# Kernel tuning notes

Hardware: AMD Instinct MI355X
Metric: run time of the kernel (lower is better)

The kernel has to match this reference:

```python
import jax, jax.numpy as jnp
import numpy as np

N_INST = 131072      # total patches across all bags
D_EMB = 512          # VGG16 pooling='max' output dim
ATT_UNITS = 128
CLS_UNITS = 512
NUM_BAGS = 256


def setup_inputs() -> dict:
    key = jax.random.key(0)
    ks = jax.random.split(key, 16)
    first_emb = jax.random.normal(ks[0], (N_INST, D_EMB), dtype=jnp.float32)
    first_lab = jnp.sort(jax.random.randint(ks[1], (N_INST,), 0, NUM_BAGS)).astype(jnp.int64)
    s = 0.02
    return {
        "first_emb": first_emb,
        "first_lab": first_lab,
        # first-level attention head: Dense(tanh) -> Dense(1, sigmoid)
        "W_a1": jax.random.normal(ks[2], (D_EMB, ATT_UNITS), dtype=jnp.float32) * s,
        "b_a1": jnp.zeros((ATT_UNITS,), dtype=jnp.float32),
        "w_o1": jax.random.normal(ks[3], (ATT_UNITS, 1), dtype=jnp.float32) * s,
        "b_o1": jnp.zeros((1,), dtype=jnp.float32),
        # second-level attention head
        "W_a2": jax.random.normal(ks[4], (D_EMB, ATT_UNITS), dtype=jnp.float32) * s,
        "b_a2": jnp.zeros((ATT_UNITS,), dtype=jnp.float32),
        "w_o2": jax.random.normal(ks[5], (ATT_UNITS, 1), dtype=jnp.float32) * s,
        "b_o2": jnp.zeros((1,), dtype=jnp.float32),
        # classifier: Dense(CLS_UNITS, linear) -> Dense(1, sigmoid)
        "W_c": jax.random.normal(ks[6], (D_EMB, CLS_UNITS), dtype=jnp.float32) * s,
        "b_c": jnp.zeros((CLS_UNITS,), dtype=jnp.float32),
        "w_out": jax.random.normal(ks[7], (CLS_UNITS, 1), dtype=jnp.float32) * s,
        "b_out": jnp.zeros((1,), dtype=jnp.float32),
    }


def reference(first_emb, first_lab, W_a1, b_a1, w_o1, b_o1,
              W_a2, b_a2, w_o2, b_o2, W_c, b_c, w_out, b_out):
    # --- first-level (instance) attention ---
    a1 = jnp.tanh(first_emb @ W_a1 + b_a1)                 # [N, A]
    att1 = jax.nn.sigmoid(a1 @ w_o1 + b_o1)                # [N, 1]
    # tf: transpose(softmax(transpose(att))) == softmax over the N axis (global)
    fst_att = jax.nn.softmax(att1, axis=0)                 # [N, 1]
    # --- per-bag attention-weighted sum (fused segment reduce) ---
    # replaces the python loop of gather_nd + matmul over contiguous bags
    second_emb = jax.ops.segment_sum(fst_att * first_emb, first_lab,
                                     num_segments=NUM_BAGS)  # [B, D]
    # --- second-level (bag) attention ---
    a2 = jnp.tanh(second_emb @ W_a2 + b_a2)                # [B, A]
    att2 = jax.nn.sigmoid(a2 @ w_o2 + b_o2)                # [B, 1]
    snd_att = jax.nn.softmax(att2.T, axis=-1)              # [1, B]
    outer_bag_emb = snd_att @ second_emb                   # [1, D]
    # --- classifier (dropout is identity at inference) ---
    h = outer_bag_emb @ W_c + b_c                          # [1, CLS]
    pred = jax.nn.sigmoid(h @ w_out + b_out)               # [1, 1]
    return pred
```

## Files before the change

kernel.cpp:

```cpp
#include <hip/hip_runtime.h>
#include <cstdint>
#include <cstddef>

#define N_INST 131072
#define D_EMB  512
#define ATT    128
#define NBAGS  256
#define TILE_I 64
#define LDA    520

typedef __attribute__((ext_vector_type(8))) short  bf16x8;
typedef __attribute__((ext_vector_type(4))) float  f32x4;
typedef __attribute__((ext_vector_type(4))) unsigned short u16x4;


__device__ inline unsigned short f2b(float f) {
    unsigned u = __builtin_bit_cast(unsigned, f);
    u += 0x7FFFu + ((u >> 16) & 1u);
    return (unsigned short)(u >> 16);
}

__global__ __launch_bounds__(256) void k_prep_wt(
    const float* __restrict__ Wa1, unsigned short* __restrict__ Wt)
{
    const int n = blockIdx.x;
    for (int k = threadIdx.x; k < D_EMB; k += 256)
        Wt[(size_t)n * D_EMB + k] = f2b(Wa1[(size_t)k * ATT + n]);
}

__global__ __launch_bounds__(256, 2) void k_att1(
    const float* __restrict__ emb, const int* __restrict__ lab,
    const unsigned short* __restrict__ Wt, const float* __restrict__ ba1,
    const float* __restrict__ wo1, const float* __restrict__ bo1,
    float* __restrict__ raw, float* __restrict__ Z1)
{
    __shared__ unsigned short Ash[TILE_I * LDA];
    __shared__ float att[TILE_I];
    __shared__ float sval[TILE_I];
    __shared__ int   labs[TILE_I];

    const int t  = threadIdx.x;
    const int w  = t >> 6;
    const int l  = t & 63;
    const int l4 = l & 15;
    const int h4 = l >> 4;
    const size_t i0 = (size_t)blockIdx.x * TILE_I;

    if (t < TILE_I) { labs[t] = lab[i0 + t]; att[t] = 0.f; }

    bf16x8 bfrag[2][16];
    #pragma unroll
    for (int nt = 0; nt < 2; ++nt) {
        const int n = 16 * (2 * w + nt) + l4;
        #pragma unroll
        for (int ks = 0; ks < 16; ++ks)
            bfrag[nt][ks] = *reinterpret_cast<const bf16x8*>(
                &Wt[(size_t)n * D_EMB + 32 * ks + 8 * h4]);
    }

    float ba1v[2], wo1v[2];
    #pragma unroll
    for (int nt = 0; nt < 2; ++nt) {
        int c = 16 * (2 * w + nt) + l4;
        ba1v[nt] = ba1[c];
        wo1v[nt] = wo1[c];
    }

    #pragma unroll
    for (int g = 0; g < 4; ++g) {
        float4 v[8];
        #pragma unroll
        for (int j = 0; j < 8; ++j) {
            int idx = (g * 8 + j) * 256 + t;
            int row = idx >> 7;
            int c4  = (idx & 127) * 4;
            v[j] = *reinterpret_cast<const float4*>(&emb[(i0 + row) * D_EMB + c4]);
        }
        #pragma unroll
        for (int j = 0; j < 8; ++j) {
            int idx = (g * 8 + j) * 256 + t;
            int row = idx >> 7;
            int c4  = (idx & 127) * 4;
            u16x4 b = { f2b(v[j].x), f2b(v[j].y), f2b(v[j].z), f2b(v[j].w) };
            *reinterpret_cast<u16x4*>(&Ash[row * LDA + c4]) = b;
        }
    }
    __syncthreads();

    f32x4 acc[4][2];
    #pragma unroll
    for (int rt = 0; rt < 4; ++rt) {
        acc[rt][0] = (f32x4){0.f, 0.f, 0.f, 0.f};
        acc[rt][1] = (f32x4){0.f, 0.f, 0.f, 0.f};
    }
    #pragma unroll
    for (int rt = 0; rt < 4; ++rt) {
        #pragma unroll
        for (int ks = 0; ks < 16; ++ks) {
            bf16x8 af = *reinterpret_cast<const bf16x8*>(
                &Ash[(16 * rt + l4) * LDA + 32 * ks + 8 * h4]);
            acc[rt][0] = __builtin_amdgcn_mfma_f32_16x16x32_bf16(
                af, bfrag[0][ks], acc[rt][0], 0, 0, 0);
            acc[rt][1] = __builtin_amdgcn_mfma_f32_16x16x32_bf16(
                af, bfrag[1][ks], acc[rt][1], 0, 0, 0);
        }
    }

    #pragma unroll
    for (int rt = 0; rt < 4; ++rt) {
        #pragma unroll
        for (int reg = 0; reg < 4; ++reg) {
            float p = tanhf(acc[rt][0][reg] + ba1v[0]) * wo1v[0]
                    + tanhf(acc[rt][1][reg] + ba1v[1]) * wo1v[1];
            p += __shfl_xor(p, 1);
            p += __shfl_xor(p, 2);
            p += __shfl_xor(p, 4);
            p += __shfl_xor(p, 8);
            if (l4 == 0) atomicAdd(&att[16 * rt + 4 * h4 + reg], p);
        }
    }
    __syncthreads();
    if (t < TILE_I) {
        float a  = att[t] + bo1[0];
        float sg = 1.f / (1.f + __expf(-a));
        sval[t]  = __expf(sg);
    }
    __syncthreads();
    if (t < TILE_I) {
        float z = sval[t];
        #pragma unroll
        for (int m = 1; m < 64; m <<= 1) z += __shfl_xor(z, m);
        if (t == 0) atomicAdd(Z1, z);
    }

    int s0 = 0;
    while (s0 < TILE_I) {
        int bag = labs[s0];
        int s1 = s0 + 1;
        while (s1 < TILE_I && labs[s1] == bag) ++s1;
        float a0 = 0.f, a1 = 0.f;
        #pragma unroll 8
        for (int ii = s0; ii < s1; ++ii) {
            unsigned u = *reinterpret_cast<const unsigned*>(
                &Ash[(size_t)ii * LDA + 2 * t]);
            float lo = __builtin_bit_cast(float, u << 16);
            float hi = __builtin_bit_cast(float, u & 0xffff0000u);
            float s  = sval[ii];
            a0 = fmaf(s, lo, a0);
            a1 = fmaf(s, hi, a1);
        }
        atomicAdd(&raw[bag * D_EMB + 2 * t], a0);
        atomicAdd(&raw[bag * D_EMB + 2 * t + 1], a1);
        s0 = s1;
    }
}

__global__ __launch_bounds__(128) void k_att2(
    const float* __restrict__ Wa2, const float* __restrict__ ba2,
    const float* __restrict__ wo2, const float* __restrict__ bo2,
    float* __restrict__ raw, const float* __restrict__ Z1,
    float* __restrict__ e2, float* __restrict__ Z2)
{
    __shared__ float sec[D_EMB];
    __shared__ float hh[2];
    const int b = blockIdx.x;
    const int t = threadIdx.x;
    const float zinv = 1.f / Z1[0];
    for (int d = t; d < D_EMB; d += 128) {
        float v = raw[b * D_EMB + d] * zinv;
        raw[b * D_EMB + d] = v;
        sec[d] = v;
    }
    __syncthreads();
    float dot = 0.f;
    #pragma unroll 8
    for (int d = 0; d < D_EMB; ++d) dot = fmaf(sec[d], Wa2[d * ATT + t], dot);
    float h = tanhf(dot + ba2[t]) * wo2[t];
    #pragma unroll
    for (int m = 1; m < 64; m <<= 1) h += __shfl_xor(h, m);
    if ((t & 63) == 0) hh[t >> 6] = h;
    __syncthreads();
    if (t == 0) {
        float a  = hh[0] + hh[1] + bo2[0];
        float sg = 1.f / (1.f + __expf(-a));
        float e  = __expf(sg);
        e2[b] = e;
        atomicAdd(Z2, e);
    }
}

__global__ __launch_bounds__(256) void k_v(
    const float* __restrict__ Wc, const float* __restrict__ wout,
    float* __restrict__ v)
{
    const int t   = threadIdx.x;
    const int row = blockIdx.x * 8 + (t >> 5);
    const int l   = t & 31;
    float s = 0.f;
    #pragma unroll 4
    for (int c = l; c < 512; c += 32) s = fmaf(Wc[(size_t)row * 512 + c], wout[c], s);
    #pragma unroll
    for (int m = 1; m < 32; m <<= 1) s += __shfl_xor(s, m);
    if (l == 0) v[row] = s;
}

__global__ __launch_bounds__(256) void k_pool(
    const float* __restrict__ raw, const float* __restrict__ e2,
    float* __restrict__ outer)
{
    const int t  = threadIdx.x;
    const int b0 = blockIdx.x * 32;
    float o0 = 0.f, o1 = 0.f;
    for (int b = b0; b < b0 + 32; ++b) {
        float wgt = e2[b];
        float2 r = *reinterpret_cast<const float2*>(&raw[b * D_EMB + 2 * t]);
        o0 = fmaf(wgt, r.x, o0);
        o1 = fmaf(wgt, r.y, o1);
    }
    atomicAdd(&outer[2 * t], o0);
    atomicAdd(&outer[2 * t + 1], o1);
}

__global__ __launch_bounds__(256) void k_cls(
    const float* __restrict__ outer, const float* __restrict__ Z2,
    const float* __restrict__ v, const float* __restrict__ bc,
    const float* __restrict__ wout, const float* __restrict__ bout,
    float* __restrict__ out)
{
    __shared__ float pp[4];
    const int t = threadIdx.x;
    const float z2inv = 1.f / Z2[0];
    float p = (outer[2 * t] * v[2 * t] + outer[2 * t + 1] * v[2 * t + 1]) * z2inv
            + bc[2 * t] * wout[2 * t] + bc[2 * t + 1] * wout[2 * t + 1];
    #pragma unroll
    for (int m = 1; m < 64; m <<= 1) p += __shfl_xor(p, m);
    if ((t & 63) == 0) pp[t >> 6] = p;
    __syncthreads();
    if (t == 0) {
        float s = pp[0] + pp[1] + pp[2] + pp[3] + bout[0];
        out[0] = 1.f / (1.f + __expf(-s));
    }
}

extern "C" void kernel_launch(void* const* d_in, const int* in_sizes, int n_in,
                              void* d_out, int out_size, void* d_ws, size_t ws_size,
                              hipStream_t stream)
{
    const float* emb  = (const float*)d_in[0];
    const int*   lab  = (const int*)d_in[1];
    const float* Wa1  = (const float*)d_in[2];
    const float* ba1  = (const float*)d_in[3];
    const float* wo1  = (const float*)d_in[4];
    const float* bo1  = (const float*)d_in[5];
    const float* Wa2  = (const float*)d_in[6];
    const float* ba2  = (const float*)d_in[7];
    const float* wo2  = (const float*)d_in[8];
    const float* bo2  = (const float*)d_in[9];
    const float* Wc   = (const float*)d_in[10];
    const float* bc   = (const float*)d_in[11];
    const float* wout = (const float*)d_in[12];
    const float* bout = (const float*)d_in[13];

    float* ws    = (float*)d_ws;
    float* Z1    = ws + 0;
    float* Z2    = ws + 1;
    float* v     = ws + 16;
    float* e2    = ws + 1024;
    float* outer = ws + 1536;
    float* raw   = ws + 2048;
    unsigned short* Wt = (unsigned short*)(ws + 133120);

    hipMemsetAsync(d_ws, 0, (size_t)(2048 + NBAGS * D_EMB) * sizeof(float), stream);

    hipLaunchKernelGGL(k_prep_wt, dim3(ATT),             dim3(256), 0, stream, Wa1, Wt);
    hipLaunchKernelGGL(k_v,       dim3(64),              dim3(256), 0, stream, Wc, wout, v);
    hipLaunchKernelGGL(k_att1,    dim3(N_INST / TILE_I), dim3(256), 0, stream,
                       emb, lab, Wt, ba1, wo1, bo1, raw, Z1);
    hipLaunchKernelGGL(k_att2,    dim3(NBAGS),           dim3(128), 0, stream,
                       Wa2, ba2, wo2, bo2, raw, Z1, e2, Z2);
    hipLaunchKernelGGL(k_pool,    dim3(8),               dim3(256), 0, stream,
                       raw, e2, outer);
    hipLaunchKernelGGL(k_cls,     dim3(1),               dim3(256), 0, stream,
                       outer, Z2, v, bc, wout, bout, (float*)d_out);
}
```

Before: 140.3 us.

## Replicate per-bag accumulators to cut atomic contention, use fast tanh

```diff
diff --git a/kernel.cpp b/kernel.cpp
--- a/kernel.cpp
+++ b/kernel.cpp
@@ -20,6 +20,11 @@
     return (unsigned short)(u >> 16);
 }
 
+__device__ inline float fast_tanh(float x) {
+    float e = __expf(2.f * x);
+    return 1.f - 2.f / (e + 1.f);
+}
+
 __global__ __launch_bounds__(256) void k_prep_wt(
     const float* __restrict__ Wa1, unsigned short* __restrict__ Wt)
 {
@@ -32,10 +37,10 @@
     const float* __restrict__ emb, const int* __restrict__ lab,
     const unsigned short* __restrict__ Wt, const float* __restrict__ ba1,
     const float* __restrict__ wo1, const float* __restrict__ bo1,
-    float* __restrict__ raw, float* __restrict__ Z1)
+    float* __restrict__ rawr, int R, float* __restrict__ Z1)
 {
     __shared__ unsigned short Ash[TILE_I * LDA];
-    __shared__ float att[TILE_I];
+    __shared__ float att4[4][TILE_I];
     __shared__ float sval[TILE_I];
     __shared__ int   labs[TILE_I];
 
@@ -45,8 +50,9 @@
     const int l4 = l & 15;
     const int h4 = l >> 4;
     const size_t i0 = (size_t)blockIdx.x * TILE_I;
-
-    if (t < TILE_I) { labs[t] = lab[i0 + t]; att[t] = 0.f; }
+    float* __restrict__ raw = rawr + (size_t)(blockIdx.x % R) * (NBAGS * D_EMB);
+
+    if (t < TILE_I) labs[t] = lab[i0 + t];
 
     bf16x8 bfrag[2][16];
     #pragma unroll
@@ -67,18 +73,18 @@
     }
 
     #pragma unroll
-    for (int g = 0; g < 4; ++g) {
-        float4 v[8];
-        #pragma unroll
-        for (int j = 0; j < 8; ++j) {
-            int idx = (g * 8 + j) * 256 + t;
+    for (int g = 0; g < 2; ++g) {
+        float4 v[16];
+        #pragma unroll
+        for (int j = 0; j < 16; ++j) {
+            int idx = (g * 16 + j) * 256 + t;
             int row = idx >> 7;
             int c4  = (idx & 127) * 4;
             v[j] = *reinterpret_cast<const float4*>(&emb[(i0 + row) * D_EMB + c4]);
         }
         #pragma unroll
-        for (int j = 0; j < 8; ++j) {
-            int idx = (g * 8 + j) * 256 + t;
+        for (int j = 0; j < 16; ++j) {
+            int idx = (g * 16 + j) * 256 + t;
             int row = idx >> 7;
             int c4  = (idx & 127) * 4;
             u16x4 b = { f2b(v[j].x), f2b(v[j].y), f2b(v[j].z), f2b(v[j].w) };
@@ -110,18 +116,18 @@
     for (int rt = 0; rt < 4; ++rt) {
         #pragma unroll
         for (int reg = 0; reg < 4; ++reg) {
-            float p = tanhf(acc[rt][0][reg] + ba1v[0]) * wo1v[0]
-                    + tanhf(acc[rt][1][reg] + ba1v[1]) * wo1v[1];
+            float p = fast_tanh(acc[rt][0][reg] + ba1v[0]) * wo1v[0]
+                    + fast_tanh(acc[rt][1][reg] + ba1v[1]) * wo1v[1];
             p += __shfl_xor(p, 1);
             p += __shfl_xor(p, 2);
             p += __shfl_xor(p, 4);
             p += __shfl_xor(p, 8);
-            if (l4 == 0) atomicAdd(&att[16 * rt + 4 * h4 + reg], p);
+            if (l4 == 0) att4[w][16 * rt + 4 * h4 + reg] = p;
         }
     }
     __syncthreads();
     if (t < TILE_I) {
-        float a  = att[t] + bo1[0];
+        float a  = att4[0][t] + att4[1][t] + att4[2][t] + att4[3][t] + bo1[0];
         float sg = 1.f / (1.f + __expf(-a));
         sval[t]  = __expf(sg);
     }
@@ -158,7 +164,7 @@
 __global__ __launch_bounds__(128) void k_att2(
     const float* __restrict__ Wa2, const float* __restrict__ ba2,
     const float* __restrict__ wo2, const float* __restrict__ bo2,
-    float* __restrict__ raw, const float* __restrict__ Z1,
+    float* __restrict__ rawr, int R, const float* __restrict__ Z1,
     float* __restrict__ e2, float* __restrict__ Z2)
 {
     __shared__ float sec[D_EMB];
@@ -167,15 +173,18 @@
     const int t = threadIdx.x;
     const float zinv = 1.f / Z1[0];
     for (int d = t; d < D_EMB; d += 128) {
-        float v = raw[b * D_EMB + d] * zinv;
-        raw[b * D_EMB + d] = v;
+        float s = 0.f;
+        for (int r = 0; r < R; ++r)
+            s += rawr[(size_t)r * (NBAGS * D_EMB) + b * D_EMB + d];
+        float v = s * zinv;
+        rawr[b * D_EMB + d] = v;
         sec[d] = v;
     }
     __syncthreads();
     float dot = 0.f;
     #pragma unroll 8
     for (int d = 0; d < D_EMB; ++d) dot = fmaf(sec[d], Wa2[d * ATT + t], dot);
-    float h = tanhf(dot + ba2[t]) * wo2[t];
+    float h = fast_tanh(dot + ba2[t]) * wo2[t];
     #pragma unroll
     for (int m = 1; m < 64; m <<= 1) h += __shfl_xor(h, m);
     if ((t & 63) == 0) hh[t >> 6] = h;
@@ -267,19 +276,22 @@
     float* v     = ws + 16;
     float* e2    = ws + 1024;
     float* outer = ws + 1536;
-    float* raw   = ws + 2048;
-    unsigned short* Wt = (unsigned short*)(ws + 133120);
-
-    hipMemsetAsync(d_ws, 0, (size_t)(2048 + NBAGS * D_EMB) * sizeof(float), stream);
+    unsigned short* Wt = (unsigned short*)(ws + 4096);
+    float* rawr  = ws + 36864;
+
+    const size_t need8 = ((size_t)36864 + 8u * NBAGS * D_EMB) * sizeof(float);
+    const int R = (ws_size >= need8) ? 8 : 1;
+
+    hipMemsetAsync(d_ws, 0, ((size_t)36864 + (size_t)R * NBAGS * D_EMB) * sizeof(float), stream);
 
     hipLaunchKernelGGL(k_prep_wt, dim3(ATT),             dim3(256), 0, stream, Wa1, Wt);
     hipLaunchKernelGGL(k_v,       dim3(64),              dim3(256), 0, stream, Wc, wout, v);
     hipLaunchKernelGGL(k_att1,    dim3(N_INST / TILE_I), dim3(256), 0, stream,
-                       emb, lab, Wt, ba1, wo1, bo1, raw, Z1);
+                       emb, lab, Wt, ba1, wo1, bo1, rawr, R, Z1);
     hipLaunchKernelGGL(k_att2,    dim3(NBAGS),           dim3(128), 0, stream,
-                       Wa2, ba2, wo2, bo2, raw, Z1, e2, Z2);
+                       Wa2, ba2, wo2, bo2, rawr, R, Z1, e2, Z2);
     hipLaunchKernelGGL(k_pool,    dim3(8),               dim3(256), 0, stream,
-                       raw, e2, outer);
+                       rawr, e2, outer);
     hipLaunchKernelGGL(k_cls,     dim3(1),               dim3(256), 0, stream,
                        outer, Z2, v, bc, wout, bout, (float*)d_out);
 }
```

Measured after the change: 141.2 us. Within noise of the previous version (+0.6%).
